# Performance work log

Measured on AMD Instinct MI355X. Metric: run time of the kernel, lower is better.

Reference implementation:

```python
import jax, jax.numpy as jnp
import numpy as np
from jax.scipy.linalg import solve_triangular

B, S, H, D, L = 8, 256, 768, 128, 64


def setup_inputs() -> dict:
    key = jax.random.key(0)
    ks = jax.random.split(key, 14)
    f = lambda k, shp, s=1.0: (jax.random.normal(k, shp, dtype=jnp.float32) * s)
    return {
        'word_feat_mean': f(ks[0], (B, S, H)),
        'word_feat_div': f(ks[1], (B, S, H)),
        'sent_feat_mean': f(ks[2], (B, 1, H)),
        'sent_feat_div': f(ks[3], (B, 1, H)),
        'W1': f(ks[4], (H, D), 0.02), 'b1': f(ks[5], (D,), 0.02),
        'W2': f(ks[6], (H, D), 0.02), 'b2': f(ks[7], (D,), 0.02),
        'W3': f(ks[8], (H, D), 0.02), 'b3': f(ks[9], (D,), 0.02),
        'W4': f(ks[10], (H, D), 0.02), 'b4': f(ks[11], (D,), 0.02),
        'label_mean': f(ks[12], (L, D)),
        'label_div_vec': f(ks[13], (L, D)),
    }


def _jsd_rank1(mu_p, v_p, mu_q, v_q):
    """Symmetric Gaussian JSD (0.5*(KL12+KL21)) between N(mu_p, I+v_p v_p^T) (labels, [L,D])
    and N(mu_q, I+v_q v_q^T) (words, [B,S,D]) via Sherman-Morrison closed form -> [B,L,S].
    Same math as torch.distributions MVN KL with Sigma = I + vv^T."""
    d = mu_p.shape[-1]
    n_p = 1.0 + jnp.sum(v_p * v_p, -1)            # [L]   = det(I+vp vp^T)
    n_q = 1.0 + jnp.sum(v_q * v_q, -1)            # [B,S]
    dot = jnp.einsum('ld,bsd->bls', v_p, v_q)     # vp.vq
    # ||mu_q - mu_p||^2 expanded without materializing [B,L,S,D]
    d2 = (jnp.sum(mu_q * mu_q, -1)[:, None, :]
          - 2.0 * jnp.einsum('ld,bsd->bls', mu_p, mu_q)
          + jnp.sum(mu_p * mu_p, -1)[None, :, None])
    vq_delta = (jnp.einsum('bsd,bsd->bs', v_q, mu_q)[:, None, :]
                - jnp.einsum('ld,bsd->bls', mu_p, v_q))
    vp_delta = (jnp.einsum('ld,bsd->bls', v_p, mu_q)
                - jnp.sum(v_p * mu_p, -1)[None, :, None])
    n_p_b = n_p[None, :, None]
    n_q_b = n_q[:, None, :]
    maha_q = d2 - vq_delta ** 2 / n_q_b           # delta^T Sigma_q^{-1} delta
    maha_p = d2 - vp_delta ** 2 / n_p_b
    tr_pq = d + (n_p_b - 1.0) - ((n_q_b - 1.0) + dot ** 2) / n_q_b  # tr(Sq^{-1} Sp)
    tr_qp = d + (n_q_b - 1.0) - ((n_p_b - 1.0) + dot ** 2) / n_p_b
    kl_pq = 0.5 * (jnp.log(n_q_b) - jnp.log(n_p_b) - d + tr_pq + maha_q)
    kl_qp = 0.5 * (jnp.log(n_p_b) - jnp.log(n_q_b) - d + tr_qp + maha_p)
    return 0.5 * (kl_pq + kl_qp)


def _jsd_full(mu_p, S_p, mu_q, S_q):
    """Symmetric JSD between full-covariance Gaussians, Cholesky-based (like torch MVN KL).
    mu_*: [..., D], S_*: [..., D, D] -> [...]."""
    d = mu_p.shape[-1]
    L_p = jnp.linalg.cholesky(S_p)
    L_q = jnp.linalg.cholesky(S_q)
    logdet_p = 2.0 * jnp.sum(jnp.log(jnp.diagonal(L_p, axis1=-2, axis2=-1)), -1)
    logdet_q = 2.0 * jnp.sum(jnp.log(jnp.diagonal(L_q, axis1=-2, axis2=-1)), -1)
    delta = mu_q - mu_p

    def kl(La, Lb, logda, logdb):
        # KL(a||b) = 0.5*(logdet_b - logdet_a - d + tr(Sb^{-1}Sa) + delta^T Sb^{-1} delta)
        X = solve_triangular(Lb, La, lower=True)
        tr = jnp.sum(X * X, axis=(-1, -2))
        y = solve_triangular(Lb, delta[..., None], lower=True)[..., 0]
        maha = jnp.sum(y * y, -1)
        return 0.5 * (logdb - logda - d + tr + maha)

    return 0.5 * (kl(L_p, L_q, logdet_p, logdet_q) + kl(L_q, L_p, logdet_q, logdet_p))


def reference(word_feat_mean, word_feat_div, sent_feat_mean, sent_feat_div,
              W1, b1, W2, b2, W3, b3, W4, b4, label_mean, label_div_vec):
    Bx, Sx, _ = word_feat_mean.shape
    Dx = W1.shape[1]
    Lx = label_mean.shape[0]
    wm = word_feat_mean @ W1 + b1        # jw1: [B,S,D]
    wv = word_feat_div @ W2 + b2         # jw2: [B,S,D]
    sm = sent_feat_mean @ W3 + b3        # jw3: [B,1,D]
    sv = sent_feat_div @ W4 + b4         # jw4: [B,1,D]
    eye = jnp.eye(Dx, dtype=wm.dtype)
    # Gaussian JSD attention: q = labels, k = v = words (closed-form, no [B,L*S,D,D])
    score = jax.nn.softmax(_jsd_rank1(label_mean, label_div_vec, wm, wv), axis=-1)  # [B,L,S]
    v_mean = jnp.einsum('bls,bsd->bld', score, wm)
    word_cov = eye + wv[..., :, None] * wv[..., None, :]                 # [B,S,D,D]
    v_div = jnp.einsum('bls,bsde->blde', score, word_cov)                # [B,L,D,D]
    sent_cov = eye + sv[..., :, None] * sv[..., None, :]                 # [B,1,D,D]
    text_mean = (sm + v_mean) / 2                                        # [B,L,D]
    text_div = (sent_cov + v_div) / 2                                    # [B,L,D,D]
    label_cov = eye + label_div_vec[:, :, None] * label_div_vec[:, None, :]  # [L,D,D]
    lm_b = jnp.broadcast_to(label_mean, (Bx, Lx, Dx))
    lc_b = jnp.broadcast_to(label_cov, (Bx, Lx, Dx, Dx))
    relate_score = _jsd_full(text_mean, text_div, lm_b, lc_b)            # [B,L]
    return relate_score, lm_b, lc_b
```

## Files before the change

kernel.cpp:

```cpp
#include <hip/hip_runtime.h>
#include <hip/hip_bf16.h>


#define PITCH 132

typedef __attribute__((ext_vector_type(8))) short bf16x8;
typedef __attribute__((ext_vector_type(4))) float f32x4;

__device__ __forceinline__ float bf2f(unsigned int u) {
    union { unsigned int i; float f; } c; c.i = u << 16; return c.f;
}
__device__ __forceinline__ unsigned short f2bf(float f) {
    __hip_bfloat16 h = __float2bfloat16(f);
    union { __hip_bfloat16 h; unsigned short u; } c; c.h = h; return c.u;
}

__global__ __launch_bounds__(256, 2)
void k1_gemm(const float* __restrict__ Am, const float* __restrict__ Av,
             const float* __restrict__ sfm, const float* __restrict__ sfd,
             const float* __restrict__ W1, const float* __restrict__ B1,
             const float* __restrict__ W2, const float* __restrict__ B2,
             const float* __restrict__ W3, const float* __restrict__ B3,
             const float* __restrict__ W4, const float* __restrict__ B4,
             float* __restrict__ wm, float* __restrict__ wv,
             float* __restrict__ sm, float* __restrict__ sv,
             unsigned short* __restrict__ wvTg) {
    __shared__ float At[8][64];
    __shared__ __align__(16) float Wt[64][128];
    __shared__ float tileT[8][129];
    const int tid = threadIdx.x;
    const int sel = blockIdx.y;
    const bool sentB = (blockIdx.x == 256);
    const float* A  = sentB ? (sel ? sfd : sfm) : (sel ? Av : Am);
    const float* W  = sentB ? (sel ? W4 : W3) : (sel ? W2 : W1);
    const float* Bs = sentB ? (sel ? B4 : B3) : (sel ? B2 : B1);
    float* D = sentB ? (sel ? sv : sm) : (sel ? wv : wm);
    const int R0 = sentB ? 0 : blockIdx.x * 8;
    const int r = tid >> 5;
    const int j0 = (tid & 31) * 4;
    float acc[4] = {0.f, 0.f, 0.f, 0.f};
    for (int k0 = 0; k0 < 768; k0 += 64) {
        __syncthreads();
        {
            int f = tid;
            At[f >> 6][f & 63] = A[(size_t)(R0 + (f >> 6)) * 768 + k0 + (f & 63)];
            f = tid + 256;
            At[f >> 6][f & 63] = A[(size_t)(R0 + (f >> 6)) * 768 + k0 + (f & 63)];
        }
#pragma unroll
        for (int it = 0; it < 8; ++it) {
            int f = tid + it * 256;
            int rr = f >> 5, c4 = (f & 31) * 4;
            *(float4*)&Wt[rr][c4] = *(const float4*)&W[(size_t)(k0 + rr) * 128 + c4];
        }
        __syncthreads();
#pragma unroll 16
        for (int kk = 0; kk < 64; ++kk) {
            float a = At[r][kk];
            float4 w0 = *(const float4*)&Wt[kk][j0];
            acc[0] += a * w0.x; acc[1] += a * w0.y; acc[2] += a * w0.z; acc[3] += a * w0.w;
        }
    }
    {
        float b0 = Bs[j0], b1 = Bs[j0 + 1], b2 = Bs[j0 + 2], b3 = Bs[j0 + 3];
        float4 o = make_float4(acc[0] + b0, acc[1] + b1, acc[2] + b2, acc[3] + b3);
        *(float4*)&D[(size_t)(R0 + r) * 128 + j0] = o;
        tileT[r][j0 + 0] = o.x; tileT[r][j0 + 1] = o.y;
        tileT[r][j0 + 2] = o.z; tileT[r][j0 + 3] = o.w;
    }
    if (sel && !sentB) {
        __syncthreads();
        if (tid < 128) {
            int d = tid;
            unsigned short u[8];
#pragma unroll
            for (int ss = 0; ss < 8; ++ss) u[ss] = f2bf(tileT[ss][d]);
            unsigned int p0 = (unsigned int)u[0] | ((unsigned int)u[1] << 16);
            unsigned int p1 = (unsigned int)u[2] | ((unsigned int)u[3] << 16);
            unsigned int p2 = (unsigned int)u[4] | ((unsigned int)u[5] << 16);
            unsigned int p3 = (unsigned int)u[6] | ((unsigned int)u[7] << 16);
            unsigned short* dst = wvTg + (size_t)(R0 >> 8) * 32768 + (size_t)d * 256 + (R0 & 255);
            *(uint4*)dst = make_uint4(p0, p1, p2, p3);
        }
    }
}

template <int N>
__device__ __forceinline__ void bsumN(float* v, float* red) {
#pragma unroll
    for (int o = 32; o; o >>= 1)
#pragma unroll
        for (int n = 0; n < N; ++n) v[n] += __shfl_xor(v[n], o);
    __syncthreads();
    if ((threadIdx.x & 63) == 0) {
        int w = threadIdx.x >> 6;
#pragma unroll
        for (int n = 0; n < N; ++n) red[w * N + n] = v[n];
    }
    __syncthreads();
#pragma unroll
    for (int n = 0; n < N; ++n)
        v[n] = red[0 * N + n] + red[1 * N + n] + red[2 * N + n] + red[3 * N + n];
    __syncthreads();
}

__global__ __launch_bounds__(256, 2)
void k4_fused(const float* __restrict__ wm, const float* __restrict__ wv,
              const unsigned short* __restrict__ wvTg,
              const float* __restrict__ smg, const float* __restrict__ svg,
              const float* __restrict__ lmg, const float* __restrict__ ldvg,
              float* __restrict__ out) {
    extern __shared__ float smem[];
    float* Amat = smem;
    float* Wb   = smem + 16896;
    float* Sbuf = Wb;
    float* ssq  = smem + 19008;
    float* svr  = smem + 19264;
    float* vrow = smem + 19392;
    float* zv   = smem + 19520;
    float* zd   = smem + 19648;
    float* red  = smem + 19776;
    float* scoreL = Amat;
    float* vpart  = Amat + 256;

    const int tid = threadIdx.x;
    const int bid = blockIdx.x;
    const int b = bid >> 6, l = bid & 63;

    if (tid < 128) {
        svr[tid]  = svg[b * 128 + tid];
        vrow[tid] = ldvg[l * 128 + tid];
        zv[tid]   = lmg[l * 128 + tid];
    }
    __syncthreads();
    if (tid < 32) {
        float4 v = *(const float4*)&lmg[l * 128 + tid * 4];
        *(float4*)&out[512 + (size_t)bid * 128 + tid * 4] = v;
    }
    {
        float* lcb = out + 512 + 65536 + (size_t)bid * 16384;
#pragma unroll
        for (int q = 0; q < 16; ++q) {
            int flat4 = q * 256 + tid;
            int i = flat4 >> 5;
            int j4 = (flat4 & 31) * 4;
            float vi = vrow[i];
            float4 r;
            r.x = vi * vrow[j4 + 0] + ((i == j4 + 0) ? 1.f : 0.f);
            r.y = vi * vrow[j4 + 1] + ((i == j4 + 1) ? 1.f : 0.f);
            r.z = vi * vrow[j4 + 2] + ((i == j4 + 2) ? 1.f : 0.f);
            r.w = vi * vrow[j4 + 3] + ((i == j4 + 3) ? 1.f : 0.f);
            *(float4*)&lcb[(size_t)flat4 * 4] = r;
        }
    }
    float lv[3] = {0.f, 0.f, 0.f};
    if (tid < 128) {
        float m = zv[tid], v = vrow[tid];
        lv[0] = m * m; lv[1] = v * v; lv[2] = m * v;
    }
    bsumN<3>(lv, red);
    const float mmp = lv[0], np = 1.f + lv[1], vmp = lv[2];
    const float4* wmr = (const float4*)(wm + (size_t)(b * 256 + tid) * 128);
    const float4* wvr = (const float4*)(wv + (size_t)(b * 256 + tid) * 128);
    float md = 0.f, dot = 0.f, pvv = 0.f, vq = 0.f;
    float smm = 0.f, svv = 0.f, smv = 0.f;
#pragma unroll 8
    for (int q = 0; q < 32; ++q) {
        float4 xm = wmr[q], xv = wvr[q];
        const float* m4 = &zv[q * 4];
        const float* v4 = &vrow[q * 4];
        md  += m4[0] * xm.x + m4[1] * xm.y + m4[2] * xm.z + m4[3] * xm.w;
        dot += v4[0] * xv.x + v4[1] * xv.y + v4[2] * xv.z + v4[3] * xv.w;
        pvv += m4[0] * xv.x + m4[1] * xv.y + m4[2] * xv.z + m4[3] * xv.w;
        vq  += v4[0] * xm.x + v4[1] * xm.y + v4[2] * xm.z + v4[3] * xm.w;
        smm += xm.x * xm.x + xm.y * xm.y + xm.z * xm.z + xm.w * xm.w;
        svv += xv.x * xv.x + xv.y * xv.y + xv.z * xv.z + xv.w * xv.w;
        smv += xm.x * xv.x + xm.y * xv.y + xm.z * xv.z + xm.w * xv.w;
    }
    float nq = 1.f + svv;
    float d2 = smm - 2.f * md + mmp;
    float vqd = smv - pvv, vpd = vq - vmp;
    float inq = 1.f / nq, inp = 1.f / np;
    float maha_q = d2 - vqd * vqd * inq;
    float maha_p = d2 - vpd * vpd * inp;
    float logit = 0.25f * ((np - 1.f) + (nq - 1.f)
                           - (nq - 1.f + dot * dot) * inq
                           - (np - 1.f + dot * dot) * inp
                           + maha_q + maha_p);
    float mx = logit;
#pragma unroll
    for (int o = 32; o; o >>= 1) mx = fmaxf(mx, __shfl_xor(mx, o));
    if ((tid & 63) == 0) red[tid >> 6] = mx;
    __syncthreads();
    mx = fmaxf(fmaxf(red[0], red[1]), fmaxf(red[2], red[3]));
    float e = expf(logit - mx);
    float s = e;
#pragma unroll
    for (int o = 32; o; o >>= 1) s += __shfl_xor(s, o);
    __syncthreads();
    if ((tid & 63) == 0) red[tid >> 6] = s;
    __syncthreads();
    float tot = red[0] + red[1] + red[2] + red[3];
    float sc = e / tot;
    scoreL[tid] = sc;
    ssq[tid] = sqrtf(sc);
    __syncthreads();
    {
        int d4 = (tid & 31) * 4, sg = tid >> 5;
        const float* wmb = wm + (size_t)b * 256 * 128;
        float ax = 0.f, ay = 0.f, az = 0.f, aw = 0.f;
        for (int s2 = sg * 32; s2 < sg * 32 + 32; ++s2) {
            float w = scoreL[s2];
            float4 x = *(const float4*)&wmb[(size_t)s2 * 128 + d4];
            ax += w * x.x; ay += w * x.y; az += w * x.z; aw += w * x.w;
        }
        *(float4*)&vpart[sg * 128 + d4] = make_float4(ax, ay, az, aw);
    }
    __syncthreads();
    if (tid < 128) {
        float vm8 = 0.f;
#pragma unroll
        for (int g2 = 0; g2 < 8; ++g2) vm8 += vpart[g2 * 128 + tid];
        zd[tid] = zv[tid] - 0.5f * (smg[b * 128 + tid] + vm8);
        zv[tid] = vrow[tid];
    }
    __syncthreads();
    {
        unsigned short* Sb = (unsigned short*)Amat;
        const unsigned short* src = wvTg + (size_t)b * 32768;
        const int s0 = (tid & 31) * 8;
        float ssv[8];
#pragma unroll
        for (int j = 0; j < 8; ++j) ssv[j] = ssq[s0 + j];
#pragma unroll
        for (int it = 0; it < 16; ++it) {
            int f8 = tid + it * 256;
            int d = f8 >> 5;
            uint4 raw = *(const uint4*)&src[(size_t)f8 * 8];
            unsigned int p0 = (unsigned int)f2bf(bf2f(raw.x & 0xffffu) * ssv[0])
                            | ((unsigned int)f2bf(bf2f(raw.x >> 16) * ssv[1]) << 16);
            unsigned int p1 = (unsigned int)f2bf(bf2f(raw.y & 0xffffu) * ssv[2])
                            | ((unsigned int)f2bf(bf2f(raw.y >> 16) * ssv[3]) << 16);
            unsigned int p2 = (unsigned int)f2bf(bf2f(raw.z & 0xffffu) * ssv[4])
                            | ((unsigned int)f2bf(bf2f(raw.z >> 16) * ssv[5]) << 16);
            unsigned int p3 = (unsigned int)f2bf(bf2f(raw.w & 0xffffu) * ssv[6])
                            | ((unsigned int)f2bf(bf2f(raw.w >> 16) * ssv[7]) << 16);
            *(uint4*)&Sb[(size_t)d * 264 + s0] = make_uint4(p0, p1, p2, p3);
        }
    }
    __syncthreads();
    {
        const unsigned short* Sb = (const unsigned short*)Amat;
        const int w = tid >> 6, ln = tid & 63;
        const int rl = ln & 15, g = ln >> 4;
        const int arow0 = 16 * w + rl;
        const int arow1 = 16 * (w + 4) + rl;
        f32x4 acc0[8], acc1[8];
#pragma unroll
        for (int t = 0; t < 8; ++t) {
            acc0[t] = (f32x4){0.f, 0.f, 0.f, 0.f};
            acc1[t] = (f32x4){0.f, 0.f, 0.f, 0.f};
        }
#pragma unroll
        for (int ks = 0; ks < 8; ++ks) {
            bf16x8 a0 = *(const bf16x8*)&Sb[(size_t)arow0 * 264 + ks * 32 + g * 8];
            bf16x8 a1 = *(const bf16x8*)&Sb[(size_t)arow1 * 264 + ks * 32 + g * 8];
#pragma unroll
            for (int tj = 0; tj < 8; ++tj) {
                bf16x8 bb = *(const bf16x8*)&Sb[(size_t)(16 * tj + rl) * 264 + ks * 32 + g * 8];
                acc0[tj] = __builtin_amdgcn_mfma_f32_16x16x32_bf16(a0, bb, acc0[tj], 0, 0, 0);
                acc1[tj] = __builtin_amdgcn_mfma_f32_16x16x32_bf16(a1, bb, acc1[tj], 0, 0, 0);
            }
        }
        __syncthreads();
#pragma unroll
        for (int tj = 0; tj < 8; ++tj) {
            int j = 16 * tj + rl;
            float svj = svr[j];
#pragma unroll
            for (int r = 0; r < 4; ++r) {
                int i = 16 * w + g * 4 + r;
                Amat[i * PITCH + j] = ((i == j) ? 1.f : 0.f) + 0.5f * (svr[i] * svj + acc0[tj][r]);
                int i2 = 16 * (w + 4) + g * 4 + r;
                Amat[i2 * PITCH + j] = ((i2 == j) ? 1.f : 0.f) + 0.5f * (svr[i2] * svj + acc1[tj][r]);
            }
        }
    }
    __syncthreads();
    float v5[5] = {0.f, 0.f, 0.f, 0.f, 0.f};
    if (tid < 128) {
        v5[0] = Amat[tid * PITCH + tid];
        float vv = vrow[tid], de = zd[tid];
        v5[1] = vv * vv; v5[2] = de * de; v5[3] = vv * de;
    }
    {
        int i = tid >> 1, h = tid & 1;
        const float* Ar = &Amat[i * PITCH + h * 64];
        const float* vr = &vrow[h * 64];
        float s2 = 0.f;
        for (int k2 = 0; k2 < 64; k2 += 4) {
            float4 a = *(const float4*)&Ar[k2];
            s2 += a.x * vr[k2] + a.y * vr[k2 + 1] + a.z * vr[k2 + 2] + a.w * vr[k2 + 3];
        }
        v5[4] = vrow[i] * s2;
    }
    bsumN<5>(v5, red);
    const float trP = v5[0], nv = v5[1], dds = v5[2], vds = v5[3], vsv = v5[4];
    for (int p = 0; p < 8; ++p) {
        const int base = 16 * p;
        const int R = 112 - base;
        __syncthreads();
        if (p > 0) {
            const int pb = base - 16;
            if (tid >= base && tid < 128) {
                int i = tid;
                const float* Lr = &Amat[i * PITCH + pb];
                float dv = 0.f, dd2 = 0.f;
#pragma unroll
                for (int t = 0; t < 16; ++t) {
                    float lvv = Lr[t];
                    dv  += lvv * zv[pb + t];
                    dd2 += lvv * zd[pb + t];
                }
                zv[i] -= dv; zd[i] -= dd2;
            }
            int njobs = (R + 16) * 16;
            for (int idx = tid; idx < njobs; idx += 256) {
                int r2 = idx >> 4, jc = idx & 15;
                int i = base + r2, j = base + jc;
                if (j <= i) {
                    const float* wi = &Wb[i];
                    const float* wj = &Wb[j];
                    float acc2 = 0.f;
#pragma unroll
                    for (int t2 = 0; t2 < 16; ++t2)
                        acc2 += wi[t2 * PITCH] * wj[t2 * PITCH];
                    Amat[i * PITCH + j] -= acc2;
                }
            }
        }
        __syncthreads();
        if (tid < 64) {
            const int c = tid;
            float cv[16];
            if (c < 16) {
#pragma unroll
                for (int r2 = 0; r2 < 16; ++r2) {
                    int hi = (r2 >= c) ? r2 : c, lo2 = (r2 >= c) ? c : r2;
                    cv[r2] = Amat[(base + hi) * PITCH + base + lo2];
                }
            } else {
#pragma unroll
                for (int r2 = 0; r2 < 16; ++r2) cv[r2] = 0.f;
            }
#pragma unroll
            for (int t = 0; t < 16; ++t) {
                float lt[16];
#pragma unroll
                for (int r2 = 0; r2 < 16; ++r2) lt[r2] = __shfl(cv[r2], t);
                float invs = 1.f / sqrtf(lt[t]);
                if (c == t) {
#pragma unroll
                    for (int r2 = 0; r2 < 16; ++r2) cv[r2] = (r2 >= t) ? lt[r2] * invs : 0.f;
                } else if (c > t && c < 16) {
                    float lc = lt[c] * invs;
#pragma unroll
                    for (int r2 = 0; r2 < 16; ++r2)
                        if (r2 > t) cv[r2] -= (lt[r2] * invs) * lc;
                }
            }
            float x[16], acb[16];
#pragma unroll
            for (int r2 = 0; r2 < 16; ++r2) acb[r2] = 0.f;
#pragma unroll
            for (int r2 = 0; r2 < 16; ++r2) {
                float Lrr = __shfl(cv[r2], r2);
                float xr = (((c == r2) ? 1.f : 0.f) - acb[r2]) / Lrr;
                x[r2] = xr;
#pragma unroll
                for (int q = r2 + 1; q < 16; ++q) acb[q] += __shfl(cv[q], r2) * xr;
            }
            if (c < 16) {
#pragma unroll
                for (int r2 = 0; r2 < 16; ++r2)
                    Amat[(base + c) * PITCH + base + r2] = x[r2];
            }
            if (c < 32) {
                int t2 = c & 15;
                float* zp = (c < 16) ? zv : zd;
                float a0 = 0.f;
#pragma unroll
                for (int a = 0; a < 16; ++a)
                    a0 += Amat[(base + a) * PITCH + base + t2] * zp[base + a];
                zp[base + t2] = a0;
            }
        } else if (p > 0 && R > 0) {
            int nt = R >> 3;
            int ntri = (nt * (nt + 1)) >> 1;
            for (int tau = tid - 64; tau < ntri; tau += 192) {
                float ft = sqrtf(8.f * (float)tau + 1.f);
                int tr = (int)((ft - 1.f) * 0.5f);
                while (((tr + 1) * (tr + 2)) / 2 <= tau) ++tr;
                while ((tr * (tr + 1)) / 2 > tau) --tr;
                int tc = tau - ((tr * (tr + 1)) >> 1);
                int ii = base + 16 + tr * 8, jj = base + 16 + tc * 8;
                float a2[8][8];
#pragma unroll
                for (int r2 = 0; r2 < 8; ++r2)
#pragma unroll
                    for (int c2 = 0; c2 < 8; ++c2) a2[r2][c2] = 0.f;
#pragma unroll
                for (int t = 0; t < 16; ++t) {
                    const float* wr = &Wb[t * PITCH];
                    float4 x0 = *(const float4*)&wr[ii];
                    float4 x1 = *(const float4*)&wr[ii + 4];
                    float4 y0 = *(const float4*)&wr[jj];
                    float4 y1 = *(const float4*)&wr[jj + 4];
                    float xa[8] = {x0.x,x0.y,x0.z,x0.w, x1.x,x1.y,x1.z,x1.w};
                    float yb[8] = {y0.x,y0.y,y0.z,y0.w, y1.x,y1.y,y1.z,y1.w};
#pragma unroll
                    for (int r2 = 0; r2 < 8; ++r2)
#pragma unroll
                        for (int c2 = 0; c2 < 8; ++c2) a2[r2][c2] += xa[r2] * yb[c2];
                }
#pragma unroll
                for (int r2 = 0; r2 < 8; ++r2) {
                    float* Ar2 = &Amat[(ii + r2) * PITCH + jj];
                    float4 u0 = *(float4*)&Ar2[0];
                    float4 u1 = *(float4*)&Ar2[4];
                    u0.x -= a2[r2][0]; u0.y -= a2[r2][1]; u0.z -= a2[r2][2]; u0.w -= a2[r2][3];
                    u1.x -= a2[r2][4]; u1.y -= a2[r2][5]; u1.z -= a2[r2][6]; u1.w -= a2[r2][7];
                    *(float4*)&Ar2[0] = u0;
                    *(float4*)&Ar2[4] = u1;
                }
            }
        }
        __syncthreads();
        if (R > 0 && tid < R) {
            int i = base + 16 + tid;
            const float* Ar = &Amat[i * PITCH + base];
            float4 q0 = *(const float4*)&Ar[0];
            float4 q1 = *(const float4*)&Ar[4];
            float4 q2 = *(const float4*)&Ar[8];
            float4 q3 = *(const float4*)&Ar[12];
            float rA[16] = {q0.x,q0.y,q0.z,q0.w, q1.x,q1.y,q1.z,q1.w,
                            q2.x,q2.y,q2.z,q2.w, q3.x,q3.y,q3.z,q3.w};
            float lo[16];
#pragma unroll
            for (int t = 0; t < 16; ++t) lo[t] = 0.f;
#pragma unroll
            for (int a = 0; a < 16; ++a) {
                float va = rA[a];
                const float* Trow = &Amat[(base + a) * PITCH + base];
                float4 t0 = *(const float4*)&Trow[0];
                float4 t1 = *(const float4*)&Trow[4];
                float4 t2 = *(const float4*)&Trow[8];
                float4 t3 = *(const float4*)&Trow[12];
                lo[0] += va * t0.x; lo[1] += va * t0.y; lo[2] += va * t0.z; lo[3] += va * t0.w;
                lo[4] += va * t1.x; lo[5] += va * t1.y; lo[6] += va * t1.z; lo[7] += va * t1.w;
                lo[8] += va * t2.x; lo[9] += va * t2.y; lo[10] += va * t2.z; lo[11] += va * t2.w;
                lo[12] += va * t3.x; lo[13] += va * t3.y; lo[14] += va * t3.z; lo[15] += va * t3.w;
            }
            float* Aw = &Amat[i * PITCH + base];
            *(float4*)&Aw[0]  = make_float4(lo[0], lo[1], lo[2], lo[3]);
            *(float4*)&Aw[4]  = make_float4(lo[4], lo[5], lo[6], lo[7]);
            *(float4*)&Aw[8]  = make_float4(lo[8], lo[9], lo[10], lo[11]);
            *(float4*)&Aw[12] = make_float4(lo[12], lo[13], lo[14], lo[15]);
#pragma unroll
            for (int t = 0; t < 16; ++t) Wb[t * PITCH + i] = lo[t];
        }
    }
    for (int s2 = 1; s2 <= 7; ++s2) {
        __syncthreads();
        int npair = 8 - s2;
        int jobs = npair * 16;
        int len = 16 * s2;
        for (int t = tid; t < jobs; t += 256) {
            int pr = t >> 4;
            int ta = (t >> 2) & 3, tb = t & 3;
            int i = pr + s2, J = pr;
            const float* u0 = &Amat[(16 * i + ta * 4) * PITCH + 16 * J];
            const float* w0 = &Amat[(16 * J + tb * 4) * PITCH + 16 * J];
            float a4[4][4];
#pragma unroll
            for (int r2 = 0; r2 < 4; ++r2)
#pragma unroll
                for (int c2 = 0; c2 < 4; ++c2) a4[r2][c2] = 0.f;
            for (int k = 0; k < len; k += 4) {
                float4 ur[4], wr4[4];
#pragma unroll
                for (int r2 = 0; r2 < 4; ++r2) ur[r2] = *(const float4*)&u0[r2 * PITCH + k];
#pragma unroll
                for (int c2 = 0; c2 < 4; ++c2) wr4[c2] = *(const float4*)&w0[c2 * PITCH + k];
#pragma unroll
                for (int r2 = 0; r2 < 4; ++r2)
#pragma unroll
                    for (int c2 = 0; c2 < 4; ++c2)
                        a4[r2][c2] += ur[r2].x * wr4[c2].x + ur[r2].y * wr4[c2].y
                                    + ur[r2].z * wr4[c2].z + ur[r2].w * wr4[c2].w;
            }
#pragma unroll
            for (int r2 = 0; r2 < 4; ++r2)
#pragma unroll
                for (int c2 = 0; c2 < 4; ++c2)
                    Sbuf[pr * 256 + (ta * 4 + r2) * 16 + tb * 4 + c2] = a4[r2][c2];
        }
        __syncthreads();
        for (int idx = tid; idx < npair * 256; idx += 256) {
            int pr = idx >> 8;
            int J = pr, i = pr + s2;
            int cc = (idx >> 4) & 15, bb = idx & 15;
            float a0 = 0.f;
#pragma unroll
            for (int a = 0; a < 16; ++a)
                a0 += Amat[(16 * i + a) * PITCH + 16 * i + cc] * Sbuf[pr * 256 + a * 16 + bb];
            Amat[(16 * J + bb) * PITCH + 16 * i + cc] = -a0;
        }
    }
    __syncthreads();
    float v3[3] = {0.f, 0.f, 0.f};
    {
        int i = tid & 127, h = tid >> 7;
        int c0 = (i >> 4) << 4;
        int half = (128 - c0) >> 1;
        const float* Ar = &Amat[i * PITCH + c0 + h * half];
        for (int k2 = 0; k2 < half; k2 += 4) {
            float4 a = *(const float4*)&Ar[k2];
            v3[0] += a.x * a.x + a.y * a.y + a.z * a.z + a.w * a.w;
        }
    }
    if (tid < 128) {
        float a = zv[tid];  v3[1] = a * a;
        float d22 = zd[tid]; v3[2] = d22 * d22;
    }
    bsumN<3>(v3, red);
    if (tid == 0) {
        float n = 1.f + nv;
        float Aterm = trP - vsv / n;
        float Bt = v3[0] + v3[1];
        float mq = dds - vds * vds / n;
        out[bid] = 0.25f * (Aterm + Bt - 256.f + mq + v3[2]);
    }
}

extern "C" void kernel_launch(void* const* d_in, const int* in_sizes, int n_in,
                              void* d_out, int out_size, void* d_ws, size_t ws_size,
                              hipStream_t stream) {
    const float* wfm = (const float*)d_in[0];
    const float* wfd = (const float*)d_in[1];
    const float* sfm = (const float*)d_in[2];
    const float* sfd = (const float*)d_in[3];
    const float* W1 = (const float*)d_in[4];
    const float* B1 = (const float*)d_in[5];
    const float* W2 = (const float*)d_in[6];
    const float* B2 = (const float*)d_in[7];
    const float* W3 = (const float*)d_in[8];
    const float* B3 = (const float*)d_in[9];
    const float* W4 = (const float*)d_in[10];
    const float* B4 = (const float*)d_in[11];
    const float* lm = (const float*)d_in[12];
    const float* ldv = (const float*)d_in[13];
    float* out = (float*)d_out;
    float* ws = (float*)d_ws;

    float* wm = ws;
    float* wv = ws + 262144;
    float* sm = ws + 524288;
    float* sv = ws + 525312;
    unsigned short* wvTg = (unsigned short*)(ws + 731392);

    constexpr int SH_FLOATS = 19800;
    constexpr size_t SH_BYTES = SH_FLOATS * sizeof(float);
    (void)hipFuncSetAttribute((const void*)k4_fused,
                              hipFuncAttributeMaxDynamicSharedMemorySize,
                              (int)SH_BYTES);

    k1_gemm<<<dim3(257, 2), 256, 0, stream>>>(wfm, wfd, sfm, sfd,
                                              W1, B1, W2, B2, W3, B3, W4, B4,
                                              wm, wv, sm, sv, wvTg);
    k4_fused<<<512, 256, SH_BYTES, stream>>>(wm, wv, wvTg, sm, sv, lm, ldv, out);
}
```

Before: 190.6 us.

## Use recursive-doubling triangular inverse and precompute label norms in GEMM kernel

Replaces the seven-step sequential block-column loop for inverting the 128x128 triangular factor with a recursive doubling scheme. It inverts 32-, then 64-, then 128-sized blocks by combining already inverted diagonal halves through two small products, using fewer barriers and larger parallel steps. It also moves the per-label sums of squares and cross products into an extra block of the first kernel, replacing a block reduction in each fused block with one global load. The cost is more complex indexing and extra work in the first kernel.

```diff
diff --git a/kernel.cpp b/kernel.cpp
--- a/kernel.cpp
+++ b/kernel.cpp
@@ -22,14 +22,36 @@
              const float* __restrict__ W2, const float* __restrict__ B2,
              const float* __restrict__ W3, const float* __restrict__ B3,
              const float* __restrict__ W4, const float* __restrict__ B4,
+             const float* __restrict__ lm, const float* __restrict__ ldv,
              float* __restrict__ wm, float* __restrict__ wv,
              float* __restrict__ sm, float* __restrict__ sv,
+             float4* __restrict__ labscg,
              unsigned short* __restrict__ wvTg) {
+    const int tid = threadIdx.x;
+    const int sel = blockIdx.y;
+    if (blockIdx.x == 257) {
+        if (sel == 0) {
+            int l = tid >> 2, q = tid & 3;
+            const float* mr = lm + (size_t)l * 128 + q * 32;
+            const float* vr = ldv + (size_t)l * 128 + q * 32;
+            float s0 = 0.f, s1 = 0.f, s2 = 0.f;
+            for (int k = 0; k < 32; k += 4) {
+                float4 m = *(const float4*)&mr[k];
+                float4 v = *(const float4*)&vr[k];
+                s0 += m.x * m.x + m.y * m.y + m.z * m.z + m.w * m.w;
+                s1 += v.x * v.x + v.y * v.y + v.z * v.z + v.w * v.w;
+                s2 += m.x * v.x + m.y * v.y + m.z * v.z + m.w * v.w;
+            }
+            s0 += __shfl_xor(s0, 1); s0 += __shfl_xor(s0, 2);
+            s1 += __shfl_xor(s1, 1); s1 += __shfl_xor(s1, 2);
+            s2 += __shfl_xor(s2, 1); s2 += __shfl_xor(s2, 2);
+            if (q == 0) labscg[l] = make_float4(s0, s1, s2, 0.f);
+        }
+        return;
+    }
     __shared__ float At[8][64];
     __shared__ __align__(16) float Wt[64][128];
     __shared__ float tileT[8][129];
-    const int tid = threadIdx.x;
-    const int sel = blockIdx.y;
     const bool sentB = (blockIdx.x == 256);
     const float* A  = sentB ? (sel ? sfd : sfm) : (sel ? Av : Am);
     const float* W  = sentB ? (sel ? W4 : W3) : (sel ? W2 : W1);
@@ -109,11 +131,11 @@
               const unsigned short* __restrict__ wvTg,
               const float* __restrict__ smg, const float* __restrict__ svg,
               const float* __restrict__ lmg, const float* __restrict__ ldvg,
+              const float4* __restrict__ labscg,
               float* __restrict__ out) {
     extern __shared__ float smem[];
     float* Amat = smem;
     float* Wb   = smem + 16896;
-    float* Sbuf = Wb;
     float* ssq  = smem + 19008;
     float* svr  = smem + 19264;
     float* vrow = smem + 19392;
@@ -153,13 +175,8 @@
             *(float4*)&lcb[(size_t)flat4 * 4] = r;
         }
     }
-    float lv[3] = {0.f, 0.f, 0.f};
-    if (tid < 128) {
-        float m = zv[tid], v = vrow[tid];
-        lv[0] = m * m; lv[1] = v * v; lv[2] = m * v;
-    }
-    bsumN<3>(lv, red);
-    const float mmp = lv[0], np = 1.f + lv[1], vmp = lv[2];
+    float4 lsv = labscg[l];
+    const float mmp = lsv.x, np = 1.f + lsv.y, vmp = lsv.z;
     const float4* wmr = (const float4*)(wm + (size_t)(b * 256 + tid) * 128);
     const float4* wvr = (const float4*)(wv + (size_t)(b * 256 + tid) * 128);
     float md = 0.f, dot = 0.f, pvv = 0.f, vq = 0.f;
@@ -470,54 +487,134 @@
             for (int t = 0; t < 16; ++t) Wb[t * PITCH + i] = lo[t];
         }
     }
-    for (int s2 = 1; s2 <= 7; ++s2) {
-        __syncthreads();
-        int npair = 8 - s2;
-        int jobs = npair * 16;
-        int len = 16 * s2;
-        for (int t = tid; t < jobs; t += 256) {
-            int pr = t >> 4;
-            int ta = (t >> 2) & 3, tb = t & 3;
-            int i = pr + s2, J = pr;
-            const float* u0 = &Amat[(16 * i + ta * 4) * PITCH + 16 * J];
-            const float* w0 = &Amat[(16 * J + tb * 4) * PITCH + 16 * J];
-            float a4[4][4];
-#pragma unroll
-            for (int r2 = 0; r2 < 4; ++r2)
-#pragma unroll
-                for (int c2 = 0; c2 < 4; ++c2) a4[r2][c2] = 0.f;
-            for (int k = 0; k < len; k += 4) {
-                float4 ur[4], wr4[4];
-#pragma unroll
-                for (int r2 = 0; r2 < 4; ++r2) ur[r2] = *(const float4*)&u0[r2 * PITCH + k];
-#pragma unroll
-                for (int c2 = 0; c2 < 4; ++c2) wr4[c2] = *(const float4*)&w0[c2 * PITCH + k];
-#pragma unroll
-                for (int r2 = 0; r2 < 4; ++r2)
-#pragma unroll
-                    for (int c2 = 0; c2 < 4; ++c2)
-                        a4[r2][c2] += ur[r2].x * wr4[c2].x + ur[r2].y * wr4[c2].y
-                                    + ur[r2].z * wr4[c2].z + ur[r2].w * wr4[c2].w;
-            }
-#pragma unroll
-            for (int r2 = 0; r2 < 4; ++r2)
-#pragma unroll
-                for (int c2 = 0; c2 < 4; ++c2)
-                    Sbuf[pr * 256 + (ta * 4 + r2) * 16 + tb * 4 + c2] = a4[r2][c2];
-        }
-        __syncthreads();
-        for (int idx = tid; idx < npair * 256; idx += 256) {
-            int pr = idx >> 8;
-            int J = pr, i = pr + s2;
-            int cc = (idx >> 4) & 15, bb = idx & 15;
-            float a0 = 0.f;
-#pragma unroll
-            for (int a = 0; a < 16; ++a)
-                a0 += Amat[(16 * i + a) * PITCH + 16 * i + cc] * Sbuf[pr * 256 + a * 16 + bb];
-            Amat[(16 * J + bb) * PITCH + 16 * i + cc] = -a0;
-        }
-    }
-    __syncthreads();
+    __syncthreads();
+    for (int t = tid; t < 128; t += 256) {
+        int q = t >> 5, tt = t & 31;
+        int c0 = (tt >> 2) * 2, r0 = (tt & 3) * 4;
+        int rb = 32 * q + 16, cb = 32 * q;
+        float a4[2][4] = {{0,0,0,0},{0,0,0,0}};
+        for (int k = 0; k < 16; k += 4) {
+            float4 xc0 = *(const float4*)&Amat[(cb + c0) * PITCH + cb + k];
+            float4 xc1 = *(const float4*)&Amat[(cb + c0 + 1) * PITCH + cb + k];
+#pragma unroll
+            for (int rr = 0; rr < 4; ++rr) {
+                float4 lr = *(const float4*)&Amat[(rb + r0 + rr) * PITCH + cb + k];
+                a4[0][rr] += xc0.x * lr.x + xc0.y * lr.y + xc0.z * lr.z + xc0.w * lr.w;
+                a4[1][rr] += xc1.x * lr.x + xc1.y * lr.y + xc1.z * lr.z + xc1.w * lr.w;
+            }
+        }
+#pragma unroll
+        for (int cc = 0; cc < 2; ++cc)
+#pragma unroll
+            for (int rr = 0; rr < 4; ++rr)
+                Wb[q * 256 + (c0 + cc) * 16 + (r0 + rr)] = a4[cc][rr];
+    }
+    __syncthreads();
+    for (int t = tid; t < 128; t += 256) {
+        int q = t >> 5, tt = t & 31;
+        int c0 = (tt >> 2) * 2, r0 = (tt & 3) * 4;
+        int rb = 32 * q + 16, cb = 32 * q;
+        float a4[2][4] = {{0,0,0,0},{0,0,0,0}};
+        for (int a = 0; a < 16; ++a) {
+            float y0 = Wb[q * 256 + c0 * 16 + a];
+            float y1 = Wb[q * 256 + (c0 + 1) * 16 + a];
+            float4 t2 = *(const float4*)&Amat[(rb + a) * PITCH + rb + r0];
+            a4[0][0] += y0 * t2.x; a4[0][1] += y0 * t2.y; a4[0][2] += y0 * t2.z; a4[0][3] += y0 * t2.w;
+            a4[1][0] += y1 * t2.x; a4[1][1] += y1 * t2.y; a4[1][2] += y1 * t2.z; a4[1][3] += y1 * t2.w;
+        }
+#pragma unroll
+        for (int cc = 0; cc < 2; ++cc)
+#pragma unroll
+            for (int rr = 0; rr < 4; ++rr)
+                Amat[(cb + c0 + cc) * PITCH + rb + r0 + rr] = -a4[cc][rr];
+    }
+    __syncthreads();
+    {
+        int q = tid >> 7, tt = tid & 127;
+        int c0 = (tt >> 3) * 2, r0 = (tt & 7) * 4;
+        int rb = 64 * q + 32, cb = 64 * q;
+        int ks = c0 & ~15;
+        float a4[2][4] = {{0,0,0,0},{0,0,0,0}};
+        for (int k = ks; k < 32; k += 4) {
+            float4 xc0 = *(const float4*)&Amat[(cb + c0) * PITCH + cb + k];
+            float4 xc1 = *(const float4*)&Amat[(cb + c0 + 1) * PITCH + cb + k];
+#pragma unroll
+            for (int rr = 0; rr < 4; ++rr) {
+                float4 lr = *(const float4*)&Amat[(rb + r0 + rr) * PITCH + cb + k];
+                a4[0][rr] += xc0.x * lr.x + xc0.y * lr.y + xc0.z * lr.z + xc0.w * lr.w;
+                a4[1][rr] += xc1.x * lr.x + xc1.y * lr.y + xc1.z * lr.z + xc1.w * lr.w;
+            }
+        }
+#pragma unroll
+        for (int cc = 0; cc < 2; ++cc)
+#pragma unroll
+            for (int rr = 0; rr < 4; ++rr)
+                Wb[q * 1024 + (c0 + cc) * 32 + (r0 + rr)] = a4[cc][rr];
+    }
+    __syncthreads();
+    {
+        int q = tid >> 7, tt = tid & 127;
+        int c0 = (tt >> 3) * 2, r0 = (tt & 7) * 4;
+        int rb = 64 * q + 32, cb = 64 * q;
+        int atop = (r0 & ~15) + 15;
+        float a4[2][4] = {{0,0,0,0},{0,0,0,0}};
+        for (int a = 0; a <= atop; ++a) {
+            float y0 = Wb[q * 1024 + c0 * 32 + a];
+            float y1 = Wb[q * 1024 + (c0 + 1) * 32 + a];
+            float4 t2 = *(const float4*)&Amat[(rb + a) * PITCH + rb + r0];
+            a4[0][0] += y0 * t2.x; a4[0][1] += y0 * t2.y; a4[0][2] += y0 * t2.z; a4[0][3] += y0 * t2.w;
+            a4[1][0] += y1 * t2.x; a4[1][1] += y1 * t2.y; a4[1][2] += y1 * t2.z; a4[1][3] += y1 * t2.w;
+        }
+#pragma unroll
+        for (int cc = 0; cc < 2; ++cc)
+#pragma unroll
+            for (int rr = 0; rr < 4; ++rr)
+                Amat[(cb + c0 + cc) * PITCH + rb + r0 + rr] = -a4[cc][rr];
+    }
+    __syncthreads();
+#pragma unroll
+    for (int h3 = 0; h3 < 2; ++h3) {
+        const int ch = 32 * h3;
+        {
+            int c0 = (tid >> 4) * 2, r0 = (tid & 15) * 4;
+            int ks = (ch + c0) & ~15;
+            float a4[2][4] = {{0,0,0,0},{0,0,0,0}};
+            for (int k = ks; k < 64; k += 4) {
+                float4 xc0 = *(const float4*)&Amat[(ch + c0) * PITCH + k];
+                float4 xc1 = *(const float4*)&Amat[(ch + c0 + 1) * PITCH + k];
+#pragma unroll
+                for (int rr = 0; rr < 4; ++rr) {
+                    float4 lr = *(const float4*)&Amat[(64 + r0 + rr) * PITCH + k];
+                    a4[0][rr] += xc0.x * lr.x + xc0.y * lr.y + xc0.z * lr.z + xc0.w * lr.w;
+                    a4[1][rr] += xc1.x * lr.x + xc1.y * lr.y + xc1.z * lr.z + xc1.w * lr.w;
+                }
+            }
+#pragma unroll
+            for (int cc = 0; cc < 2; ++cc)
+#pragma unroll
+                for (int rr = 0; rr < 4; ++rr)
+                    Wb[(c0 + cc) * 64 + r0 + rr] = a4[cc][rr];
+        }
+        __syncthreads();
+        {
+            int c0 = (tid >> 4) * 2, r0 = (tid & 15) * 4;
+            int atop = (r0 & ~15) + 15;
+            float a4[2][4] = {{0,0,0,0},{0,0,0,0}};
+            for (int a = 0; a <= atop; ++a) {
+                float y0 = Wb[c0 * 64 + a];
+                float y1 = Wb[(c0 + 1) * 64 + a];
+                float4 t2 = *(const float4*)&Amat[(64 + a) * PITCH + 64 + r0];
+                a4[0][0] += y0 * t2.x; a4[0][1] += y0 * t2.y; a4[0][2] += y0 * t2.z; a4[0][3] += y0 * t2.w;
+                a4[1][0] += y1 * t2.x; a4[1][1] += y1 * t2.y; a4[1][2] += y1 * t2.z; a4[1][3] += y1 * t2.w;
+            }
+#pragma unroll
+            for (int cc = 0; cc < 2; ++cc)
+#pragma unroll
+                for (int rr = 0; rr < 4; ++rr)
+                    Amat[(ch + c0 + cc) * PITCH + 64 + r0 + rr] = -a4[cc][rr];
+        }
+        __syncthreads();
+    }
     float v3[3] = {0.f, 0.f, 0.f};
     {
         int i = tid & 127, h = tid >> 7;
@@ -567,6 +664,7 @@
     float* wv = ws + 262144;
     float* sm = ws + 524288;
     float* sv = ws + 525312;
+    float4* labscg = (float4*)(ws + 526336);
     unsigned short* wvTg = (unsigned short*)(ws + 731392);
 
     constexpr int SH_FLOATS = 19800;
@@ -575,8 +673,8 @@
                               hipFuncAttributeMaxDynamicSharedMemorySize,
                               (int)SH_BYTES);
 
-    k1_gemm<<<dim3(257, 2), 256, 0, stream>>>(wfm, wfd, sfm, sfd,
+    k1_gemm<<<dim3(258, 2), 256, 0, stream>>>(wfm, wfd, sfm, sfd,
                                               W1, B1, W2, B2, W3, B3, W4, B4,
-                                              wm, wv, sm, sv, wvTg);
-    k4_fused<<<512, 256, SH_BYTES, stream>>>(wm, wv, wvTg, sm, sv, lm, ldv, out);
+                                              lm, ldv, wm, wv, sm, sv, labscg, wvTg);
+    k4_fused<<<512, 256, SH_BYTES, stream>>>(wm, wv, wvTg, sm, sv, lm, ldv, labscg, out);
 }
```

After: 174.2 us. 1.09x faster.
